# Kernel tuning notes

Hardware: AMD Instinct MI355X
Metric: run time of the kernel (lower is better)

The kernel has to match this reference:

```python
import jax, jax.numpy as jnp
import numpy as np

B, NP, NV, E = 256, 500, 50, 128
FP, FV = 16, 16
DEG_P, DEG_V = 6, 4


def setup_inputs() -> dict:
    key = jax.random.key(0)
    ks = jax.random.split(key, 16)
    rng = np.random.default_rng(0)

    def edges(nb, n, deg):
        per = deg * n
        off = np.repeat(np.arange(nb, dtype=np.int32) * n, per)
        ei = off[None, :] + rng.integers(0, n, size=(2, nb * per)).astype(np.int32)
        return jnp.asarray(ei)

    inp = {
        "p_x": jax.random.normal(ks[0], (B * NP, FP), jnp.float32),
        "v_x": jax.random.normal(ks[1], (B * NV, FV), jnp.float32),
        "p_edge_index": edges(B, NP, DEG_P),
        "v_edge_index": edges(B, NV, DEG_V),
        "p_batch": jnp.asarray(np.repeat(np.arange(B, dtype=np.int32), NP)),
        "v_batch": jnp.asarray(np.repeat(np.arange(B, dtype=np.int32), NV)),
    }

    def lin(k, fi, fo):
        s = 1.0 / np.sqrt(fi)
        kw, kb = jax.random.split(k)
        return (jax.random.uniform(kw, (fi, fo), jnp.float32, -s, s),
                jax.random.uniform(kb, (fo,), jnp.float32, -s, s))

    layers = [("pW0", "pb0", FP, E), ("pW1", "pb1", E, E), ("pW2", "pb2", E, E),
              ("vW0", "vb0", FV, E), ("vW1", "vb1", E, E), ("vW2", "vb2", E, E),
              ("hW1", "hb1", 4 * E, 2 * E), ("hW2", "hb2", 2 * E, E), ("hW3", "hb3", E, 1)]
    for j, (wn, bn, fi, fo) in enumerate(layers):
        W, b = lin(ks[2 + j], fi, fo)
        inp[wn] = W
        inp[bn] = b
    return inp


def _gcn(h, src, dst, dinv, W, b):
    # GCNConv: out[i] = sum_{j->i} dinv[j]*dinv[i] * (h[j] @ W) + dinv[i]^2 * (h[i] @ W) + b
    xw = h @ W
    msg = xw[src] * (dinv[src] * dinv[dst])[:, None]
    agg = jax.ops.segment_sum(msg, dst, num_segments=h.shape[0])
    return agg + xw * (dinv * dinv)[:, None] + b


def _encoder(x, edge_index, batch, W0, b0, W1, b1, W2, b2, nb, npg):
    N = x.shape[0]
    src, dst = edge_index[0], edge_index[1]
    h0 = x @ W0 + b0                                   # node_init_embeddings [N, E]
    ones_e = jnp.ones(src.shape[0], x.dtype)
    deg = 1.0 + jax.ops.segment_sum(ones_e, dst, num_segments=N)  # includes self loop
    dinv = jax.lax.rsqrt(deg)
    h = jax.nn.relu(_gcn(h0, src, dst, dinv, W1, b1))
    h = _gcn(h, src, dst, dinv, W2, b2)                # node_embeddings [N, E]
    counts = jax.ops.segment_sum(jnp.ones(N, x.dtype), batch, num_segments=nb)
    graph = jax.ops.segment_sum(h, batch, num_segments=nb) / counts[:, None]  # [nb, E]
    hd = h.reshape(nb, npg, -1)                        # to_dense_batch (equal-size graphs)
    h0d = h0.reshape(nb, npg, -1)
    gr = jnp.broadcast_to(graph[:, None, :], hd.shape)
    concat = jnp.concatenate([hd, h0d, gr], axis=-1)   # [nb, npg, 3E]
    mask = jnp.ones((nb, npg), bool)
    return graph, concat, mask


def reference(p_x, v_x, p_edge_index, v_edge_index, p_batch, v_batch,
              pW0, pb0, pW1, pb1, pW2, pb2,
              vW0, vb0, vW1, vb1, vW2, vb2,
              hW1, hb1, hW2, hb2, hW3, hb3):
    p_graph, _, _ = _encoder(p_x, p_edge_index, p_batch, pW0, pb0, pW1, pb1, pW2, pb2, B, NP)
    _, v_concat, v_mask = _encoder(v_x, v_edge_index, v_batch, vW0, vb0, vW1, vb1, vW2, vb2, B, NV)
    pg_rep = jnp.broadcast_to(p_graph[:, None, :], (B, NV, p_graph.shape[-1]))
    x = jnp.concatenate([v_concat, pg_rep], axis=-1)   # [B, NV, 4E]
    h = jax.nn.leaky_relu(x @ hW1 + hb1)
    h = jax.nn.leaky_relu(h @ hW2 + hb2)
    logits = (h @ hW3 + hb3)[..., 0]                   # [B, NV]
    return jnp.where(v_mask, logits, jnp.float32(-1e9))
```

## Files before the change

kernel.cpp:

```cpp
#include <hip/hip_runtime.h>
#include <hip/hip_bf16.h>

#define NP_TOT 128000
#define NV_TOT 12800
#define EP_EDGES 768000
#define EV_EDGES 51200
#define NB 256
#define PEPG 3000
#define VEPG 200
#define VCAP 24
#define PITCHV 138

typedef short bf16x8 __attribute__((ext_vector_type(8)));
typedef float f32x4 __attribute__((ext_vector_type(4)));

static __device__ __forceinline__ unsigned short f2bf(float f) {
    unsigned u = __builtin_bit_cast(unsigned, f);
    unsigned r = u + 0x7FFFu + ((u >> 16) & 1u);
    return (unsigned short)(r >> 16);
}
static __device__ __forceinline__ float bf2f(unsigned short h) {
    return __builtin_bit_cast(float, (unsigned)h << 16);
}

static __device__ __forceinline__ void frag_elem(const float* __restrict__ W,
                                                 short* __restrict__ Fh,
                                                 short* __restrict__ Fl,
                                                 int K, int M, int e) {
    if (e >= K * M) return;
    int col = e % M, kk = e / M;
    int ks = kk >> 5, rem = kk & 31, fq = rem >> 3, j = rem & 7;
    float v = W[(size_t)kk * M + col];
    unsigned short h = f2bf(v);
    size_t dst = (((size_t)col * (K >> 5) + ks) * 4 + fq) * 8 + j;
    Fh[dst] = (short)h;
    Fl[dst] = (short)f2bf(v - bf2f(h));
}

__global__ __launch_bounds__(256) void prep_k(
    const float* __restrict__ pW0, const float* __restrict__ pb0,
    const float* __restrict__ pW1,
    float* __restrict__ W01, float* __restrict__ b01,
    const float* __restrict__ vW1, short* __restrict__ W1vh, short* __restrict__ W1vl,
    const float* __restrict__ vW2, short* __restrict__ W2vh, short* __restrict__ W2vl,
    const float* __restrict__ hW1, short* __restrict__ H1h, short* __restrict__ H1l,
    const float* __restrict__ hW2, short* __restrict__ H2h, short* __restrict__ H2l) {
    int bid = blockIdx.x, t = threadIdx.x;
    if (bid == 0) {
        if (t < 128) {
            int col = t;
            float acc[17];
            #pragma unroll
            for (int r = 0; r < 17; r++) acc[r] = 0.f;
            for (int i = 0; i < 128; i++) {
                float w1 = pW1[i * 128 + col];
                #pragma unroll
                for (int r = 0; r < 16; r++) acc[r] += pW0[r * 128 + i] * w1;
                acc[16] += pb0[i] * w1;
            }
            #pragma unroll
            for (int r = 0; r < 16; r++) W01[r * 128 + col] = acc[r];
            b01[col] = acc[16];
        }
    } else if (bid < 65) {
        frag_elem(vW1, W1vh, W1vl, 128, 128, (bid - 1) * 256 + t);
    } else if (bid < 129) {
        frag_elem(vW2, W2vh, W2vl, 128, 128, (bid - 65) * 256 + t);
    } else if (bid < 641) {
        frag_elem(hW1, H1h, H1l, 512, 256, (bid - 129) * 256 + t);
    } else {
        frag_elem(hW2, H2h, H2l, 256, 128, (bid - 641) * 256 + t);
    }
}

__global__ __launch_bounds__(512) void pfused3(const float* __restrict__ x,
                                               const int* __restrict__ ei,
                                               const float* __restrict__ W01,
                                               const float* __restrict__ b01,
                                               const float* __restrict__ b1,
                                               float* __restrict__ p_gz) {
    __shared__ char lds[77824];
    float* sx = (float*)lds;
    unsigned short* sadj = (unsigned short*)(lds + 34816);
    char*  zb    = lds + 59392;
    float* sdinv = (float*)(lds + 69632);
    int*   scnt  = (int*)(lds + 71680);
    float* sbeta = (float*)(lds + 73728);
    float* scsum = (float*)(lds + 75776);

    const int t = threadIdx.x;
    const int b = blockIdx.x;

    scnt[t] = 0; scsum[t] = 0.f;
    const float4* x4 = (const float4*)(x + (size_t)b * 500 * 16);
    for (int i = t; i < 2000; i += 512) {
        float4 v = x4[i];
        int n = i >> 2, q = i & 3;
        float* dst = &sx[n * 17 + q * 4];
        dst[0] = v.x; dst[1] = v.y; dst[2] = v.z; dst[3] = v.w;
    }
    __syncthreads();

    const int* esrc = ei + (size_t)b * PEPG;
    const int* edst = ei + EP_EDGES + (size_t)b * PEPG;
    const int base = b * 500;

    for (int e = t; e < PEPG; e += 512) {
        int s = esrc[e] - base, d = edst[e] - base;
        int slot = atomicAdd(&scnt[d], 1);
        if (slot < VCAP) sadj[d * VCAP + slot] = (unsigned short)s;
    }
    __syncthreads();
    sdinv[t] = rsqrtf(1.0f + (float)scnt[t]);
    __syncthreads();

    for (int e = t; e < PEPG; e += 512)
        atomicAdd(&scsum[esrc[e] - base], sdinv[edst[e] - base]);
    __syncthreads();
    scsum[t] = (t < 500) ? sdinv[t] * (sdinv[t] + scsum[t]) * (1.0f / 500.0f) : 0.f;

    const int lane = t & 63;
    const int wvi = t >> 6;
    const int fr = lane & 15;
    const int fq = lane >> 4;
    const int col = wvi * 16 + fr;
    bf16x8 B1, B2;
    {
        float wt[8];
        #pragma unroll
        for (int j = 0; j < 8; j++)
            wt[j] = W01[(size_t)((fq * 8 + j) & 15) * 128 + col];
        short b1a[8], b2a[8];
        #pragma unroll
        for (int j = 0; j < 8; j++) {
            int kk = fq * 8 + j;
            unsigned short h = f2bf(wt[j]);
            b1a[j] = (short)h;
            b2a[j] = (kk < 16) ? (short)f2bf(wt[j] - bf2f(h)) : (short)0;
        }
        B1 = (bf16x8){b1a[0],b1a[1],b1a[2],b1a[3],b1a[4],b1a[5],b1a[6],b1a[7]};
        B2 = (bf16x8){b2a[0],b2a[1],b2a[2],b2a[3],b2a[4],b2a[5],b2a[6],b2a[7]};
    }
    float b01c = b01[col];
    float b1c = b1[col];
    float pools = 0.f;

    const int cg = t & 7, nb_ = t >> 3, c0 = cg * 2;
    #pragma unroll
    for (int ch = 0; ch < 4; ch++) {
        __syncthreads();
        #pragma unroll
        for (int pass = 0; pass < 2; pass++) {
            int n = ch * 128 + pass * 64 + nb_;
            char* zr = zb + (pass * 64 + nb_) * 80 + cg * 4;
            if (n < 500) {
                float di = sdinv[n];
                int d = scnt[n]; if (d > VCAP) d = VCAP;
                const unsigned short* ap = sadj + n * VCAP;
                float a0 = 0.f, a1 = 0.f, ts = 0.f;
                for (int e = 0; e < d; e++) {
                    int jl = ap[e];
                    float dj = sdinv[jl];
                    a0 += dj * sx[jl * 17 + c0];
                    a1 += dj * sx[jl * 17 + c0 + 1];
                    ts += dj;
                }
                float z0 = di * (di * sx[n * 17 + c0] + a0);
                float z1 = di * (di * sx[n * 17 + c0 + 1] + a1);
                unsigned short h0 = f2bf(z0), h1 = f2bf(z1);
                unsigned short l0 = f2bf(z0 - bf2f(h0)), l1 = f2bf(z1 - bf2f(h1));
                *(unsigned*)(zr)      = (unsigned)h0 | ((unsigned)h1 << 16);
                *(unsigned*)(zr + 32) = (unsigned)l0 | ((unsigned)l1 << 16);
                if (cg == 0) sbeta[n] = di * (di + ts);
            } else {
                *(unsigned*)(zr) = 0u;
                *(unsigned*)(zr + 32) = 0u;
                if (cg == 0) sbeta[n] = 0.f;
            }
        }
        __syncthreads();
        f32x4 acc[8];
        #pragma unroll
        for (int m = 0; m < 8; m++) acc[m] = (f32x4){0.f, 0.f, 0.f, 0.f};
        #pragma unroll
        for (int m = 0; m < 8; m++) {
            int rl = m * 16 + fr;
            bf16x8 a = *(bf16x8*)(zb + rl * 80 + fq * 16);
            acc[m] = __builtin_amdgcn_mfma_f32_16x16x32_bf16(a, B1, acc[m], 0, 0, 0);
            acc[m] = __builtin_amdgcn_mfma_f32_16x16x32_bf16(a, B2, acc[m], 0, 0, 0);
        }
        #pragma unroll
        for (int m = 0; m < 8; m++)
            #pragma unroll
            for (int j = 0; j < 4; j++) {
                int rl = ch * 128 + m * 16 + fq * 4 + j;
                float v = fmaxf(acc[m][j] + sbeta[rl] * b01c + b1c, 0.f);
                pools += scsum[rl] * v;
            }
    }
    pools += __shfl_xor(pools, 16);
    pools += __shfl_xor(pools, 32);
    if (fq == 0) p_gz[(size_t)b * 128 + col] = pools;
}

#define LB 0
#define LC 35328
#define LD 68096
#define LE 100864
#define E_SDINV (LE)
#define E_SCNT  (LE + 256)
#define E_SADJ  (LE + 512)
#define E_SVG   (LE + 5376)
#define E_VGH   (LE + 5888)
#define E_VGL   (LE + 6144)
#define E_PGH   (LE + 6400)
#define E_PGL   (LE + 6656)
#define E_WSUM  (LE + 6912)
__global__ __launch_bounds__(512) void vhead_k(
    const float* __restrict__ v_x,
    const int* __restrict__ v_ei,
    const float* __restrict__ W0, const float* __restrict__ b0,
    const short* __restrict__ W1h, const short* __restrict__ W1l,
    const float* __restrict__ b1,
    const short* __restrict__ W2h, const short* __restrict__ W2l,
    const float* __restrict__ b2,
    const float* __restrict__ p_gz,
    const float* __restrict__ pW2, const float* __restrict__ pb2,
    const short* __restrict__ H1h, const short* __restrict__ H1l,
    const float* __restrict__ hb1,
    const short* __restrict__ H2h, const short* __restrict__ H2l,
    const float* __restrict__ hb2,
    const float* __restrict__ w3, const float* __restrict__ b3,
    float* __restrict__ out) {
    __shared__ char lds[109824];
    const int t = threadIdx.x;
    const int b = blockIdx.x;
    const int lane = t & 63;
    const int wv = t >> 6;
    const int fr = lane & 15;
    const int fq = lane >> 4;
    float* Bf = (float*)(lds + LB);
    float* sdinv = (float*)(lds + E_SDINV);
    int*   scnt  = (int*)(lds + E_SCNT);
    int*   sadj  = (int*)(lds + E_SADJ);

    if (t < 64) scnt[t] = 0;
    *(float4*)(lds + LC + t * 16) = *((const float4*)W0 + t);
    {
        int col = t & 127, q = t >> 7;
        const float* gz = p_gz + (size_t)b * 128;
        float s = 0.f;
        #pragma unroll
        for (int k = 0; k < 32; k++)
            s += gz[q * 32 + k] * pW2[(size_t)(q * 32 + k) * 128 + col];
        ((float*)(lds + E_WSUM))[q * 128 + col] = s;
    }
    __syncthreads();

    if (t < VEPG) {
        int s = v_ei[b * VEPG + t] - b * 50;
        int d = v_ei[EV_EDGES + b * VEPG + t] - b * 50;
        int slot = atomicAdd(&scnt[d], 1);
        if (slot < VCAP) sadj[d * VCAP + slot] = s;
    }
    __syncthreads();

    if (t < 64)
        sdinv[t] = (t < 50) ? rsqrtf(1.0f + (float)scnt[t]) : 0.f;
    if (t < 128) {
        float* part = (float*)(lds + E_WSUM);
        float v = part[t] + part[128 + t] + part[256 + t] + part[384 + t] + pb2[t];
        unsigned short h = f2bf(v);
        ((short*)(lds + E_PGH))[t] = (short)h;
        ((short*)(lds + E_PGL))[t] = (short)f2bf(v - bf2f(h));
    }
    {
        int n = t >> 3, cg = t & 7;
        if (n < 50) {
            const float* sW0 = (const float*)(lds + LC);
            const float4* xr = (const float4*)(v_x + (size_t)(b * 50 + n) * 16);
            float4 x0 = xr[0], x1 = xr[1], x2 = xr[2], x3 = xr[3];
            float xv[16] = {x0.x,x0.y,x0.z,x0.w, x1.x,x1.y,x1.z,x1.w,
                            x2.x,x2.y,x2.z,x2.w, x3.x,x3.y,x3.z,x3.w};
            #pragma unroll
            for (int cc = 0; cc < 16; cc++) {
                int c = cg + cc * 8;
                float a = b0[c];
                #pragma unroll
                for (int k = 0; k < 16; k++) a += xv[k] * sW0[k * 128 + c];
                Bf[n * PITCHV + c] = a;
            }
        }
    }
    __syncthreads();

    {
        #pragma unroll
        for (int g = 0; g < 8; g++) {
            int r = g * 8 + wv;
            float2 v = *(const float2*)&Bf[r * PITCHV + 2 * lane];
            unsigned short h0 = f2bf(v.x), h1 = f2bf(v.y);
            unsigned short l0 = f2bf(v.x - bf2f(h0)), l1 = f2bf(v.y - bf2f(h1));
            int q = (256 + 4 * lane) ^ ((r & 7) << 4);
            *(unsigned*)(lds + LC + r * 512 + q) = (unsigned)h0 | ((unsigned)h1 << 16);
            *(unsigned*)(lds + LD + r * 512 + q) = (unsigned)l0 | ((unsigned)l1 << 16);
        }
        for (int g = 0; g < 7; g++) {
            int n = g * 8 + wv;
            if (n < 50) {
                float di = sdinv[n];
                int d = scnt[n]; if (d > VCAP) d = VCAP;
                const int* ap = sadj + n * VCAP;
                float2 a = *(const float2*)&Bf[n * PITCHV + 2 * lane];
                a.x *= di; a.y *= di;
                for (int e = 0; e < d; e++) {
                    int jl = ap[e];
                    float dj = sdinv[jl];
                    float2 v = *(const float2*)&Bf[jl * PITCHV + 2 * lane];
                    a.x += dj * v.x; a.y += dj * v.y;
                }
                float z0 = di * a.x, z1 = di * a.y;
                unsigned short h0 = f2bf(z0), h1 = f2bf(z1);
                unsigned short l0 = f2bf(z0 - bf2f(h0)), l1 = f2bf(z1 - bf2f(h1));
                int q = (4 * lane) ^ ((n & 7) << 4);
                *(unsigned*)(lds + LC + n * 512 + q) = (unsigned)h0 | ((unsigned)h1 << 16);
                *(unsigned*)(lds + LD + n * 512 + q) = (unsigned)l0 | ((unsigned)l1 << 16);
            }
        }
    }
    __syncthreads();

    {
        const int col = wv * 16 + fr;
        bf16x8 bh[4], bl[4];
        #pragma unroll
        for (int ks = 0; ks < 4; ks++) {
            int base = ((col * 4 + ks) * 4 + fq) * 8;
            bh[ks] = *(const bf16x8*)&W1h[base];
            bl[ks] = *(const bf16x8*)&W1l[base];
        }
        f32x4 acc[4];
        #pragma unroll
        for (int m = 0; m < 4; m++) acc[m] = (f32x4){0.f,0.f,0.f,0.f};
        #pragma unroll
        for (int ks = 0; ks < 4; ks++) {
            int kb = ks * 64 + fq * 16;
            #pragma unroll
            for (int m = 0; m < 4; m++) {
                int r = m * 16 + fr;
                int off = r * 512 + (kb ^ ((r & 7) << 4));
                bf16x8 ah = *(bf16x8*)(lds + LC + off);
                bf16x8 al = *(bf16x8*)(lds + LD + off);
                acc[m] = __builtin_amdgcn_mfma_f32_16x16x32_bf16(ah, bh[ks], acc[m], 0, 0, 0);
                acc[m] = __builtin_amdgcn_mfma_f32_16x16x32_bf16(ah, bl[ks], acc[m], 0, 0, 0);
                acc[m] = __builtin_amdgcn_mfma_f32_16x16x32_bf16(al, bh[ks], acc[m], 0, 0, 0);
            }
        }
        float b1c = b1[col];
        #pragma unroll
        for (int m = 0; m < 4; m++)
            #pragma unroll
            for (int j = 0; j < 4; j++) {
                int row = m * 16 + fq * 4 + j;
                Bf[row * PITCHV + col] = fmaxf(acc[m][j] + b1c, 0.f);
            }
    }
    __syncthreads();

    {
        for (int g = 0; g < 7; g++) {
            int n = g * 8 + wv;
            if (n < 50) {
                float di = sdinv[n];
                int d = scnt[n]; if (d > VCAP) d = VCAP;
                const int* ap = sadj + n * VCAP;
                float2 a = *(const float2*)&Bf[n * PITCHV + 2 * lane];
                a.x *= di; a.y *= di;
                for (int e = 0; e < d; e++) {
                    int jl = ap[e];
                    float dj = sdinv[jl];
                    float2 v = *(const float2*)&Bf[jl * PITCHV + 2 * lane];
                    a.x += dj * v.x; a.y += dj * v.y;
                }
                float z0 = di * a.x, z1 = di * a.y;
                unsigned short h0 = f2bf(z0), h1 = f2bf(z1);
                unsigned short l0 = f2bf(z0 - bf2f(h0)), l1 = f2bf(z1 - bf2f(h1));
                int q = (4 * lane) ^ ((n & 7) << 4);
                *(unsigned*)(lds + LC + n * 512 + q) = (unsigned)h0 | ((unsigned)h1 << 16);
                *(unsigned*)(lds + LD + n * 512 + q) = (unsigned)l0 | ((unsigned)l1 << 16);
            }
        }
    }
    __syncthreads();

    float h2v[4][4];
    {
        const int col = wv * 16 + fr;
        bf16x8 bh[4], bl[4];
        #pragma unroll
        for (int ks = 0; ks < 4; ks++) {
            int base = ((col * 4 + ks) * 4 + fq) * 8;
            bh[ks] = *(const bf16x8*)&W2h[base];
            bl[ks] = *(const bf16x8*)&W2l[base];
        }
        f32x4 acc[4];
        #pragma unroll
        for (int m = 0; m < 4; m++) acc[m] = (f32x4){0.f,0.f,0.f,0.f};
        #pragma unroll
        for (int ks = 0; ks < 4; ks++) {
            int kb = ks * 64 + fq * 16;
            #pragma unroll
            for (int m = 0; m < 4; m++) {
                int r = m * 16 + fr;
                int off = r * 512 + (kb ^ ((r & 7) << 4));
                bf16x8 ah = *(bf16x8*)(lds + LC + off);
                bf16x8 al = *(bf16x8*)(lds + LD + off);
                acc[m] = __builtin_amdgcn_mfma_f32_16x16x32_bf16(ah, bh[ks], acc[m], 0, 0, 0);
                acc[m] = __builtin_amdgcn_mfma_f32_16x16x32_bf16(ah, bl[ks], acc[m], 0, 0, 0);
                acc[m] = __builtin_amdgcn_mfma_f32_16x16x32_bf16(al, bh[ks], acc[m], 0, 0, 0);
            }
        }
        float b2c = b2[col];
        #pragma unroll
        for (int m = 0; m < 4; m++)
            #pragma unroll
            for (int j = 0; j < 4; j++) h2v[m][j] = acc[m][j] + b2c;
    }
    __syncthreads();

    {
        const int col = wv * 16 + fr;
        float s = 0.f;
        #pragma unroll
        for (int m = 0; m < 4; m++)
            #pragma unroll
            for (int j = 0; j < 4; j++) {
                int row = m * 16 + fq * 4 + j;
                float v = h2v[m][j];
                unsigned short h = f2bf(v);
                unsigned short l = f2bf(v - bf2f(h));
                int q = (2 * col) ^ ((row & 7) << 4);
                *(short*)(lds + LC + row * 512 + q) = (short)h;
                *(short*)(lds + LD + row * 512 + q) = (short)l;
                if (row < 50) s += v;
            }
        s += __shfl_xor(s, 16); s += __shfl_xor(s, 32);
        if (fq == 0) ((float*)(lds + E_SVG))[col] = s * (1.0f / 50.0f);
    }
    __syncthreads();

    if (t < 128) {
        float v = ((float*)(lds + E_SVG))[t];
        unsigned short h = f2bf(v);
        ((short*)(lds + E_VGH))[t] = (short)h;
        ((short*)(lds + E_VGL))[t] = (short)f2bf(v - bf2f(h));
    }
    __syncthreads();

    f32x4 accT[4][2];
    #pragma unroll
    for (int m = 0; m < 4; m++)
        #pragma unroll
        for (int nf = 0; nf < 2; nf++) accT[m][nf] = (f32x4){0.f,0.f,0.f,0.f};
    {
        #pragma unroll
        for (int ks = 0; ks < 16; ks++) {
            bf16x8 bh[2], bl[2];
            #pragma unroll
            for (int nf = 0; nf < 2; nf++) {
                int col2 = wv * 32 + nf * 16 + fr;
                int base = ((col2 * 16 + ks) * 4 + fq) * 8;
                bh[nf] = *(const bf16x8*)&H1h[base];
                bl[nf] = *(const bf16x8*)&H1l[base];
            }
            if (ks < 8) {
                int kb = ks * 64 + fq * 16;
                #pragma unroll
                for (int m = 0; m < 4; m++) {
                    int r = m * 16 + fr;
                    int off = r * 512 + (kb ^ ((r & 7) << 4));
                    bf16x8 ah = *(bf16x8*)(lds + LC + off);
                    bf16x8 al = *(bf16x8*)(lds + LD + off);
                    #pragma unroll
                    for (int nf = 0; nf < 2; nf++) {
                        accT[m][nf] = __builtin_amdgcn_mfma_f32_16x16x32_bf16(ah, bh[nf], accT[m][nf], 0, 0, 0);
                        accT[m][nf] = __builtin_amdgcn_mfma_f32_16x16x32_bf16(ah, bl[nf], accT[m][nf], 0, 0, 0);
                        accT[m][nf] = __builtin_amdgcn_mfma_f32_16x16x32_bf16(al, bh[nf], accT[m][nf], 0, 0, 0);
                    }
                }
            } else {
                int boff = (ks < 12) ? (E_VGH + (ks - 8) * 64 + fq * 16)
                                     : (E_PGH + (ks - 12) * 64 + fq * 16);
                int loff = boff + 256;
                bf16x8 ah = *(bf16x8*)(lds + boff);
                bf16x8 al = *(bf16x8*)(lds + loff);
                #pragma unroll
                for (int m = 0; m < 4; m++)
                    #pragma unroll
                    for (int nf = 0; nf < 2; nf++) {
                        accT[m][nf] = __builtin_amdgcn_mfma_f32_16x16x32_bf16(ah, bh[nf], accT[m][nf], 0, 0, 0);
                        accT[m][nf] = __builtin_amdgcn_mfma_f32_16x16x32_bf16(ah, bl[nf], accT[m][nf], 0, 0, 0);
                        accT[m][nf] = __builtin_amdgcn_mfma_f32_16x16x32_bf16(al, bh[nf], accT[m][nf], 0, 0, 0);
                    }
            }
        }
    }
    __syncthreads();
    {
        #pragma unroll
        for (int nf = 0; nf < 2; nf++) {
            int col2 = wv * 32 + nf * 16 + fr;
            float hc = hb1[col2];
            #pragma unroll
            for (int m = 0; m < 4; m++)
                #pragma unroll
                for (int j = 0; j < 4; j++) {
                    int row = m * 16 + fq * 4 + j;
                    float v = accT[m][nf][j] + hc;
                    v = v > 0.f ? v : 0.01f * v;
                    unsigned short h = f2bf(v);
                    unsigned short l = f2bf(v - bf2f(h));
                    int q = (2 * col2) ^ ((row & 7) << 4);
                    *(short*)(lds + LC + row * 512 + q) = (short)h;
                    *(short*)(lds + LD + row * 512 + q) = (short)l;
                }
        }
    }
    __syncthreads();

    {
        const int col3 = wv * 16 + fr;
        f32x4 acc[4];
        #pragma unroll
        for (int m = 0; m < 4; m++) acc[m] = (f32x4){0.f,0.f,0.f,0.f};
        #pragma unroll
        for (int ks = 0; ks < 8; ks++) {
            int base = ((col3 * 8 + ks) * 4 + fq) * 8;
            bf16x8 bh = *(const bf16x8*)&H2h[base];
            bf16x8 bl = *(const bf16x8*)&H2l[base];
            int kb = ks * 64 + fq * 16;
            #pragma unroll
            for (int m = 0; m < 4; m++) {
                int r = m * 16 + fr;
                int off = r * 512 + (kb ^ ((r & 7) << 4));
                bf16x8 ah = *(bf16x8*)(lds + LC + off);
                bf16x8 al = *(bf16x8*)(lds + LD + off);
                acc[m] = __builtin_amdgcn_mfma_f32_16x16x32_bf16(ah, bh, acc[m], 0, 0, 0);
                acc[m] = __builtin_amdgcn_mfma_f32_16x16x32_bf16(ah, bl, acc[m], 0, 0, 0);
                acc[m] = __builtin_amdgcn_mfma_f32_16x16x32_bf16(al, bh, acc[m], 0, 0, 0);
            }
        }
        float hc = hb2[col3], wc = w3[col3];
        float p[4][4];
        #pragma unroll
        for (int m = 0; m < 4; m++)
            #pragma unroll
            for (int j = 0; j < 4; j++) {
                float v = acc[m][j] + hc;
                v = v > 0.f ? v : 0.01f * v;
                p[m][j] = v * wc;
            }
        #pragma unroll
        for (int m = 0; m < 4; m++)
            #pragma unroll
            for (int j = 0; j < 4; j++) {
                p[m][j] += __shfl_xor(p[m][j], 1);
                p[m][j] += __shfl_xor(p[m][j], 2);
                p[m][j] += __shfl_xor(p[m][j], 4);
                p[m][j] += __shfl_xor(p[m][j], 8);
            }
        if (fr == 0) {
            float* wsum = (float*)(lds + E_WSUM);
            #pragma unroll
            for (int m = 0; m < 4; m++)
                #pragma unroll
                for (int j = 0; j < 4; j++)
                    wsum[wv * 64 + m * 16 + fq * 4 + j] = p[m][j];
        }
    }
    __syncthreads();
    if (t < 50) {
        float* wsum = (float*)(lds + E_WSUM);
        float s = 0.f;
        #pragma unroll
        for (int w8 = 0; w8 < 8; w8++) s += wsum[w8 * 64 + t];
        out[b * 50 + t] = s + b3[0];
    }
}

extern "C" void kernel_launch(void* const* d_in, const int* in_sizes, int n_in,
                              void* d_out, int out_size, void* d_ws, size_t ws_size,
                              hipStream_t stream) {
    const float* p_x = (const float*)d_in[0];
    const float* v_x = (const float*)d_in[1];
    const int* p_ei = (const int*)d_in[2];
    const int* v_ei = (const int*)d_in[3];
    const float* pW0 = (const float*)d_in[6];  const float* pb0 = (const float*)d_in[7];
    const float* pW1 = (const float*)d_in[8];  const float* pb1 = (const float*)d_in[9];
    const float* pW2 = (const float*)d_in[10]; const float* pb2 = (const float*)d_in[11];
    const float* vW0 = (const float*)d_in[12]; const float* vb0 = (const float*)d_in[13];
    const float* vW1 = (const float*)d_in[14]; const float* vb1 = (const float*)d_in[15];
    const float* vW2 = (const float*)d_in[16]; const float* vb2 = (const float*)d_in[17];
    const float* hW1 = (const float*)d_in[18]; const float* hb1 = (const float*)d_in[19];
    const float* hW2 = (const float*)d_in[20]; const float* hb2 = (const float*)d_in[21];
    const float* hW3 = (const float*)d_in[22]; const float* hb3 = (const float*)d_in[23];

    char* w = (char*)d_ws;
    size_t off = 0;
    auto alloc = [&](size_t bytes) { char* p = w + off; off += (bytes + 255) & ~size_t(255); return p; };
    float* p_gz = (float*)alloc((size_t)NB * 128 * 4);
    float* W01  = (float*)alloc((size_t)16 * 128 * 4);
    float* b01  = (float*)alloc((size_t)128 * 4);
    short* W1vh = (short*)alloc((size_t)128 * 128 * 2);
    short* W1vl = (short*)alloc((size_t)128 * 128 * 2);
    short* W2vh = (short*)alloc((size_t)128 * 128 * 2);
    short* W2vl = (short*)alloc((size_t)128 * 128 * 2);
    short* H1h  = (short*)alloc((size_t)512 * 256 * 2);
    short* H1l  = (short*)alloc((size_t)512 * 256 * 2);
    short* H2h  = (short*)alloc((size_t)256 * 128 * 2);
    short* H2l  = (short*)alloc((size_t)256 * 128 * 2);

    prep_k<<<769, 256, 0, stream>>>(pW0, pb0, pW1, W01, b01,
                                    vW1, W1vh, W1vl, vW2, W2vh, W2vl,
                                    hW1, H1h, H1l, hW2, H2h, H2l);
    pfused3<<<NB, 512, 0, stream>>>(p_x, p_ei, W01, b01, pb1, p_gz);
    vhead_k<<<NB, 512, 0, stream>>>(v_x, v_ei,
                                    vW0, vb0, W1vh, W1vl, vb1, W2vh, W2vl, vb2,
                                    p_gz, pW2, pb2, H1h, H1l, hb1, H2h, H2l, hb2,
                                    hW3, hb3, (float*)d_out);
}
```

Measured before the change: 83.04 us.

## Double block size to 1024 threads and split MFMA row tiles across wave halves

```diff
diff --git a/kernel.cpp b/kernel.cpp
--- a/kernel.cpp
+++ b/kernel.cpp
@@ -73,13 +73,13 @@
     }
 }
 
-__global__ __launch_bounds__(512) void pfused3(const float* __restrict__ x,
-                                               const int* __restrict__ ei,
-                                               const float* __restrict__ W01,
-                                               const float* __restrict__ b01,
-                                               const float* __restrict__ b1,
-                                               float* __restrict__ p_gz) {
-    __shared__ char lds[77824];
+__global__ __launch_bounds__(1024) void pfused3(const float* __restrict__ x,
+                                                const int* __restrict__ ei,
+                                                const float* __restrict__ W01,
+                                                const float* __restrict__ b01,
+                                                const float* __restrict__ b1,
+                                                float* __restrict__ p_gz) {
+    __shared__ char lds[78848];
     float* sx = (float*)lds;
     unsigned short* sadj = (unsigned short*)(lds + 34816);
     char*  zb    = lds + 59392;
@@ -87,13 +87,14 @@
     int*   scnt  = (int*)(lds + 71680);
     float* sbeta = (float*)(lds + 73728);
     float* scsum = (float*)(lds + 75776);
+    float* pp    = (float*)(lds + 77824);
 
     const int t = threadIdx.x;
     const int b = blockIdx.x;
 
-    scnt[t] = 0; scsum[t] = 0.f;
+    if (t < 512) { scnt[t] = 0; scsum[t] = 0.f; }
     const float4* x4 = (const float4*)(x + (size_t)b * 500 * 16);
-    for (int i = t; i < 2000; i += 512) {
+    for (int i = t; i < 2000; i += 1024) {
         float4 v = x4[i];
         int n = i >> 2, q = i & 3;
         float* dst = &sx[n * 17 + q * 4];
@@ -105,25 +106,27 @@
     const int* edst = ei + EP_EDGES + (size_t)b * PEPG;
     const int base = b * 500;
 
-    for (int e = t; e < PEPG; e += 512) {
+    for (int e = t; e < PEPG; e += 1024) {
         int s = esrc[e] - base, d = edst[e] - base;
         int slot = atomicAdd(&scnt[d], 1);
         if (slot < VCAP) sadj[d * VCAP + slot] = (unsigned short)s;
     }
     __syncthreads();
-    sdinv[t] = rsqrtf(1.0f + (float)scnt[t]);
-    __syncthreads();
-
-    for (int e = t; e < PEPG; e += 512)
+    if (t < 512) sdinv[t] = rsqrtf(1.0f + (float)scnt[t]);
+    __syncthreads();
+
+    for (int e = t; e < PEPG; e += 1024)
         atomicAdd(&scsum[esrc[e] - base], sdinv[edst[e] - base]);
     __syncthreads();
-    scsum[t] = (t < 500) ? sdinv[t] * (sdinv[t] + scsum[t]) * (1.0f / 500.0f) : 0.f;
+    if (t < 512)
+        scsum[t] = (t < 500) ? sdinv[t] * (sdinv[t] + scsum[t]) * (1.0f / 500.0f) : 0.f;
 
     const int lane = t & 63;
     const int wvi = t >> 6;
     const int fr = lane & 15;
     const int fq = lane >> 4;
-    const int col = wvi * 16 + fr;
+    const int col = (wvi & 7) * 16 + fr;
+    const int mh = (wvi >> 3) * 4;
     bf16x8 B1, B2;
     {
         float wt[8];
@@ -149,10 +152,9 @@
     #pragma unroll
     for (int ch = 0; ch < 4; ch++) {
         __syncthreads();
-        #pragma unroll
-        for (int pass = 0; pass < 2; pass++) {
-            int n = ch * 128 + pass * 64 + nb_;
-            char* zr = zb + (pass * 64 + nb_) * 80 + cg * 4;
+        {
+            int n = ch * 128 + nb_;
+            char* zr = zb + nb_ * 80 + cg * 4;
             if (n < 500) {
                 float di = sdinv[n];
                 int d = scnt[n]; if (d > VCAP) d = VCAP;
@@ -179,28 +181,30 @@
             }
         }
         __syncthreads();
-        f32x4 acc[8];
-        #pragma unroll
-        for (int m = 0; m < 8; m++) acc[m] = (f32x4){0.f, 0.f, 0.f, 0.f};
-        #pragma unroll
-        for (int m = 0; m < 8; m++) {
-            int rl = m * 16 + fr;
+        f32x4 acc[4];
+        #pragma unroll
+        for (int m = 0; m < 4; m++) acc[m] = (f32x4){0.f, 0.f, 0.f, 0.f};
+        #pragma unroll
+        for (int m = 0; m < 4; m++) {
+            int rl = (mh + m) * 16 + fr;
             bf16x8 a = *(bf16x8*)(zb + rl * 80 + fq * 16);
             acc[m] = __builtin_amdgcn_mfma_f32_16x16x32_bf16(a, B1, acc[m], 0, 0, 0);
             acc[m] = __builtin_amdgcn_mfma_f32_16x16x32_bf16(a, B2, acc[m], 0, 0, 0);
         }
         #pragma unroll
-        for (int m = 0; m < 8; m++)
+        for (int m = 0; m < 4; m++)
             #pragma unroll
             for (int j = 0; j < 4; j++) {
-                int rl = ch * 128 + m * 16 + fq * 4 + j;
+                int rl = ch * 128 + (mh + m) * 16 + fq * 4 + j;
                 float v = fmaxf(acc[m][j] + sbeta[rl] * b01c + b1c, 0.f);
                 pools += scsum[rl] * v;
             }
     }
     pools += __shfl_xor(pools, 16);
     pools += __shfl_xor(pools, 32);
-    if (fq == 0) p_gz[(size_t)b * 128 + col] = pools;
+    if (fq == 0) pp[(wvi >> 3) * 128 + col] = pools;
+    __syncthreads();
+    if (t < 128) p_gz[(size_t)b * 128 + t] = pp[t] + pp[128 + t];
 }
 
 #define LB 0
@@ -211,12 +215,12 @@
 #define E_SCNT  (LE + 256)
 #define E_SADJ  (LE + 512)
 #define E_SVG   (LE + 5376)
-#define E_VGH   (LE + 5888)
-#define E_VGL   (LE + 6144)
-#define E_PGH   (LE + 6400)
-#define E_PGL   (LE + 6656)
-#define E_WSUM  (LE + 6912)
-__global__ __launch_bounds__(512) void vhead_k(
+#define E_VGH   (LE + 6400)
+#define E_VGL   (LE + 6656)
+#define E_PGH   (LE + 6912)
+#define E_PGL   (LE + 7168)
+#define E_WSUM  (LE + 7424)
+__global__ __launch_bounds__(1024) void vhead_k(
     const float* __restrict__ v_x,
     const int* __restrict__ v_ei,
     const float* __restrict__ W0, const float* __restrict__ b0,
@@ -232,7 +236,7 @@
     const float* __restrict__ hb2,
     const float* __restrict__ w3, const float* __restrict__ b3,
     float* __restrict__ out) {
-    __shared__ char lds[109824];
+    __shared__ char lds[112384];
     const int t = threadIdx.x;
     const int b = blockIdx.x;
     const int lane = t & 63;
@@ -245,8 +249,8 @@
     int*   sadj  = (int*)(lds + E_SADJ);
 
     if (t < 64) scnt[t] = 0;
-    *(float4*)(lds + LC + t * 16) = *((const float4*)W0 + t);
-    {
+    if (t < 512) *(float4*)(lds + LC + t * 16) = *((const float4*)W0 + t);
+    if (t < 512) {
         int col = t & 127, q = t >> 7;
         const float* gz = p_gz + (size_t)b * 128;
         float s = 0.f;
@@ -296,8 +300,8 @@
 
     {
         #pragma unroll
-        for (int g = 0; g < 8; g++) {
-            int r = g * 8 + wv;
+        for (int g = 0; g < 4; g++) {
+            int r = g * 16 + wv;
             float2 v = *(const float2*)&Bf[r * PITCHV + 2 * lane];
             unsigned short h0 = f2bf(v.x), h1 = f2bf(v.y);
             unsigned short l0 = f2bf(v.x - bf2f(h0)), l1 = f2bf(v.y - bf2f(h1));
@@ -305,8 +309,8 @@
             *(unsigned*)(lds + LC + r * 512 + q) = (unsigned)h0 | ((unsigned)h1 << 16);
             *(unsigned*)(lds + LD + r * 512 + q) = (unsigned)l0 | ((unsigned)l1 << 16);
         }
-        for (int g = 0; g < 7; g++) {
-            int n = g * 8 + wv;
+        for (int g = 0; g < 4; g++) {
+            int n = g * 16 + wv;
             if (n < 50) {
                 float di = sdinv[n];
                 int d = scnt[n]; if (d > VCAP) d = VCAP;
@@ -331,7 +335,8 @@
     __syncthreads();
 
     {
-        const int col = wv * 16 + fr;
+        const int col = (wv & 7) * 16 + fr;
+        const int mh = (wv >> 3) * 2;
         bf16x8 bh[4], bl[4];
         #pragma unroll
         for (int ks = 0; ks < 4; ks++) {
@@ -339,37 +344,37 @@
             bh[ks] = *(const bf16x8*)&W1h[base];
             bl[ks] = *(const bf16x8*)&W1l[base];
         }
-        f32x4 acc[4];
-        #pragma unroll
-        for (int m = 0; m < 4; m++) acc[m] = (f32x4){0.f,0.f,0.f,0.f};
+        f32x4 acc[2];
+        acc[0] = (f32x4){0.f,0.f,0.f,0.f};
+        acc[1] = (f32x4){0.f,0.f,0.f,0.f};
         #pragma unroll
         for (int ks = 0; ks < 4; ks++) {
             int kb = ks * 64 + fq * 16;
             #pragma unroll
-            for (int m = 0; m < 4; m++) {
-                int r = m * 16 + fr;
+            for (int m2 = 0; m2 < 2; m2++) {
+                int r = (mh + m2) * 16 + fr;
                 int off = r * 512 + (kb ^ ((r & 7) << 4));
                 bf16x8 ah = *(bf16x8*)(lds + LC + off);
                 bf16x8 al = *(bf16x8*)(lds + LD + off);
-                acc[m] = __builtin_amdgcn_mfma_f32_16x16x32_bf16(ah, bh[ks], acc[m], 0, 0, 0);
-                acc[m] = __builtin_amdgcn_mfma_f32_16x16x32_bf16(ah, bl[ks], acc[m], 0, 0, 0);
-                acc[m] = __builtin_amdgcn_mfma_f32_16x16x32_bf16(al, bh[ks], acc[m], 0, 0, 0);
+                acc[m2] = __builtin_amdgcn_mfma_f32_16x16x32_bf16(ah, bh[ks], acc[m2], 0, 0, 0);
+                acc[m2] = __builtin_amdgcn_mfma_f32_16x16x32_bf16(ah, bl[ks], acc[m2], 0, 0, 0);
+                acc[m2] = __builtin_amdgcn_mfma_f32_16x16x32_bf16(al, bh[ks], acc[m2], 0, 0, 0);
             }
         }
         float b1c = b1[col];
         #pragma unroll
-        for (int m = 0; m < 4; m++)
+        for (int m2 = 0; m2 < 2; m2++)
             #pragma unroll
             for (int j = 0; j < 4; j++) {
-                int row = m * 16 + fq * 4 + j;
-                Bf[row * PITCHV + col] = fmaxf(acc[m][j] + b1c, 0.f);
-            }
-    }
-    __syncthreads();
-
-    {
-        for (int g = 0; g < 7; g++) {
-            int n = g * 8 + wv;
+                int row = (mh + m2) * 16 + fq * 4 + j;
+                Bf[row * PITCHV + col] = fmaxf(acc[m2][j] + b1c, 0.f);
+            }
+    }
+    __syncthreads();
+
+    {
+        for (int g = 0; g < 4; g++) {
+            int n = g * 16 + wv;
             if (n < 50) {
                 float di = sdinv[n];
                 int d = scnt[n]; if (d > VCAP) d = VCAP;
@@ -393,9 +398,10 @@
     }
     __syncthreads();
 
-    float h2v[4][4];
-    {
-        const int col = wv * 16 + fr;
+    float h2v[2][4];
+    {
+        const int col = (wv & 7) * 16 + fr;
+        const int mh = (wv >> 3) * 2;
         bf16x8 bh[4], bl[4];
         #pragma unroll
         for (int ks = 0; ks < 4; ks++) {
@@ -403,40 +409,41 @@
             bh[ks] = *(const bf16x8*)&W2h[base];
             bl[ks] = *(const bf16x8*)&W2l[base];
         }
-        f32x4 acc[4];
-        #pragma unroll
-        for (int m = 0; m < 4; m++) acc[m] = (f32x4){0.f,0.f,0.f,0.f};
+        f32x4 acc[2];
+        acc[0] = (f32x4){0.f,0.f,0.f,0.f};
+        acc[1] = (f32x4){0.f,0.f,0.f,0.f};
         #pragma unroll
         for (int ks = 0; ks < 4; ks++) {
             int kb = ks * 64 + fq * 16;
             #pragma unroll
-            for (int m = 0; m < 4; m++) {
-                int r = m * 16 + fr;
+            for (int m2 = 0; m2 < 2; m2++) {
+                int r = (mh + m2) * 16 + fr;
                 int off = r * 512 + (kb ^ ((r & 7) << 4));
                 bf16x8 ah = *(bf16x8*)(lds + LC + off);
                 bf16x8 al = *(bf16x8*)(lds + LD + off);
-                acc[m] = __builtin_amdgcn_mfma_f32_16x16x32_bf16(ah, bh[ks], acc[m], 0, 0, 0);
-                acc[m] = __builtin_amdgcn_mfma_f32_16x16x32_bf16(ah, bl[ks], acc[m], 0, 0, 0);
-                acc[m] = __builtin_amdgcn_mfma_f32_16x16x32_bf16(al, bh[ks], acc[m], 0, 0, 0);
+                acc[m2] = __builtin_amdgcn_mfma_f32_16x16x32_bf16(ah, bh[ks], acc[m2], 0, 0, 0);
+                acc[m2] = __builtin_amdgcn_mfma_f32_16x16x32_bf16(ah, bl[ks], acc[m2], 0, 0, 0);
+                acc[m2] = __builtin_amdgcn_mfma_f32_16x16x32_bf16(al, bh[ks], acc[m2], 0, 0, 0);
             }
         }
         float b2c = b2[col];
         #pragma unroll
-        for (int m = 0; m < 4; m++)
-            #pragma unroll
-            for (int j = 0; j < 4; j++) h2v[m][j] = acc[m][j] + b2c;
-    }
-    __syncthreads();
-
-    {
-        const int col = wv * 16 + fr;
+        for (int m2 = 0; m2 < 2; m2++)
+            #pragma unroll
+            for (int j = 0; j < 4; j++) h2v[m2][j] = acc[m2][j] + b2c;
+    }
+    __syncthreads();
+
+    {
+        const int col = (wv & 7) * 16 + fr;
+        const int mh = (wv >> 3) * 2;
         float s = 0.f;
         #pragma unroll
-        for (int m = 0; m < 4; m++)
+        for (int m2 = 0; m2 < 2; m2++)
             #pragma unroll
             for (int j = 0; j < 4; j++) {
-                int row = m * 16 + fq * 4 + j;
-                float v = h2v[m][j];
+                int row = (mh + m2) * 16 + fq * 4 + j;
+                float v = h2v[m2][j];
                 unsigned short h = f2bf(v);
                 unsigned short l = f2bf(v - bf2f(h));
                 int q = (2 * col) ^ ((row & 7) << 4);
@@ -445,30 +452,32 @@
                 if (row < 50) s += v;
             }
         s += __shfl_xor(s, 16); s += __shfl_xor(s, 32);
-        if (fq == 0) ((float*)(lds + E_SVG))[col] = s * (1.0f / 50.0f);
+        if (fq == 0) ((float*)(lds + E_SVG))[(wv >> 3) * 128 + col] = s;
     }
     __syncthreads();
 
     if (t < 128) {
-        float v = ((float*)(lds + E_SVG))[t];
+        float* svg = (float*)(lds + E_SVG);
+        float v = (svg[t] + svg[128 + t]) * (1.0f / 50.0f);
         unsigned short h = f2bf(v);
         ((short*)(lds + E_VGH))[t] = (short)h;
         ((short*)(lds + E_VGL))[t] = (short)f2bf(v - bf2f(h));
     }
     __syncthreads();
 
-    f32x4 accT[4][2];
+    f32x4 accT[2][2];
     #pragma unroll
-    for (int m = 0; m < 4; m++)
-        #pragma unroll
-        for (int nf = 0; nf < 2; nf++) accT[m][nf] = (f32x4){0.f,0.f,0.f,0.f};
-    {
+    for (int m2 = 0; m2 < 2; m2++)
+        #pragma unroll
+        for (int nf = 0; nf < 2; nf++) accT[m2][nf] = (f32x4){0.f,0.f,0.f,0.f};
+    {
+        const int mh = (wv >> 3) * 2;
         #pragma unroll
         for (int ks = 0; ks < 16; ks++) {
             bf16x8 bh[2], bl[2];
             #pragma unroll
             for (int nf = 0; nf < 2; nf++) {
-                int col2 = wv * 32 + nf * 16 + fr;
+                int col2 = (wv & 7) * 32 + nf * 16 + fr;
                 int base = ((col2 * 16 + ks) * 4 + fq) * 8;
                 bh[nf] = *(const bf16x8*)&H1h[base];
                 bl[nf] = *(const bf16x8*)&H1l[base];
@@ -476,16 +485,16 @@
             if (ks < 8) {
                 int kb = ks * 64 + fq * 16;
                 #pragma unroll
-                for (int m = 0; m < 4; m++) {
-                    int r = m * 16 + fr;
+                for (int m2 = 0; m2 < 2; m2++) {
+                    int r = (mh + m2) * 16 + fr;
                     int off = r * 512 + (kb ^ ((r & 7) << 4));
                     bf16x8 ah = *(bf16x8*)(lds + LC + off);
                     bf16x8 al = *(bf16x8*)(lds + LD + off);
                     #pragma unroll
                     for (int nf = 0; nf < 2; nf++) {
-                        accT[m][nf] = __builtin_amdgcn_mfma_f32_16x16x32_bf16(ah, bh[nf], accT[m][nf], 0, 0, 0);
-                        accT[m][nf] = __builtin_amdgcn_mfma_f32_16x16x32_bf16(ah, bl[nf], accT[m][nf], 0, 0, 0);
-                        accT[m][nf] = __builtin_amdgcn_mfma_f32_16x16x32_bf16(al, bh[nf], accT[m][nf], 0, 0, 0);
+                        accT[m2][nf] = __builtin_amdgcn_mfma_f32_16x16x32_bf16(ah, bh[nf], accT[m2][nf], 0, 0, 0);
+                        accT[m2][nf] = __builtin_amdgcn_mfma_f32_16x16x32_bf16(ah, bl[nf], accT[m2][nf], 0, 0, 0);
+                        accT[m2][nf] = __builtin_amdgcn_mfma_f32_16x16x32_bf16(al, bh[nf], accT[m2][nf], 0, 0, 0);
                     }
                 }
             } else {
@@ -495,28 +504,29 @@
                 bf16x8 ah = *(bf16x8*)(lds + boff);
                 bf16x8 al = *(bf16x8*)(lds + loff);
                 #pragma unroll
-                for (int m = 0; m < 4; m++)
+                for (int m2 = 0; m2 < 2; m2++)
                     #pragma unroll
                     for (int nf = 0; nf < 2; nf++) {
-                        accT[m][nf] = __builtin_amdgcn_mfma_f32_16x16x32_bf16(ah, bh[nf], accT[m][nf], 0, 0, 0);
-                        accT[m][nf] = __builtin_amdgcn_mfma_f32_16x16x32_bf16(ah, bl[nf], accT[m][nf], 0, 0, 0);
-                        accT[m][nf] = __builtin_amdgcn_mfma_f32_16x16x32_bf16(al, bh[nf], accT[m][nf], 0, 0, 0);
+                        accT[m2][nf] = __builtin_amdgcn_mfma_f32_16x16x32_bf16(ah, bh[nf], accT[m2][nf], 0, 0, 0);
+                        accT[m2][nf] = __builtin_amdgcn_mfma_f32_16x16x32_bf16(ah, bl[nf], accT[m2][nf], 0, 0, 0);
+                        accT[m2][nf] = __builtin_amdgcn_mfma_f32_16x16x32_bf16(al, bh[nf], accT[m2][nf], 0, 0, 0);
                     }
             }
         }
     }
     __syncthreads();
     {
+        const int mh = (wv >> 3) * 2;
         #pragma unroll
         for (int nf = 0; nf < 2; nf++) {
-            int col2 = wv * 32 + nf * 16 + fr;
+            int col2 = (wv & 7) * 32 + nf * 16 + fr;
             float hc = hb1[col2];
             #pragma unroll
-            for (int m = 0; m < 4; m++)
+            for (int m2 = 0; m2 < 2; m2++)
                 #pragma unroll
                 for (int j = 0; j < 4; j++) {
-                    int row = m * 16 + fq * 4 + j;
-                    float v = accT[m][nf][j] + hc;
+                    int row = (mh + m2) * 16 + fq * 4 + j;
+                    float v = accT[m2][nf][j] + hc;
                     v = v > 0.f ? v : 0.01f * v;
                     unsigned short h = f2bf(v);
                     unsigned short l = f2bf(v - bf2f(h));
@@ -529,10 +539,11 @@
     __syncthreads();
 
     {
-        const int col3 = wv * 16 + fr;
-        f32x4 acc[4];
-        #pragma unroll
-        for (int m = 0; m < 4; m++) acc[m] = (f32x4){0.f,0.f,0.f,0.f};
+        const int col3 = (wv & 7) * 16 + fr;
+        const int mh = (wv >> 3) * 2;
+        f32x4 acc[2];
+        acc[0] = (f32x4){0.f,0.f,0.f,0.f};
+        acc[1] = (f32x4){0.f,0.f,0.f,0.f};
         #pragma unroll
         for (int ks = 0; ks < 8; ks++) {
             int base = ((col3 * 8 + ks) * 4 + fq) * 8;
@@ -540,50 +551,51 @@
             bf16x8 bl = *(const bf16x8*)&H2l[base];
             int kb = ks * 64 + fq * 16;
             #pragma unroll
-            for (int m = 0; m < 4; m++) {
-                int r = m * 16 + fr;
+            for (int m2 = 0; m2 < 2; m2++) {
+                int r = (mh + m2) * 16 + fr;
                 int off = r * 512 + (kb ^ ((r & 7) << 4));
                 bf16x8 ah = *(bf16x8*)(lds + LC + off);
                 bf16x8 al = *(bf16x8*)(lds + LD + off);
-                acc[m] = __builtin_amdgcn_mfma_f32_16x16x32_bf16(ah, bh, acc[m], 0, 0, 0);
-                acc[m] = __builtin_amdgcn_mfma_f32_16x16x32_bf16(ah, bl, acc[m], 0, 0, 0);
-                acc[m] = __builtin_amdgcn_mfma_f32_16x16x32_bf16(al, bh, acc[m], 0, 0, 0);
+                acc[m2] = __builtin_amdgcn_mfma_f32_16x16x32_bf16(ah, bh, acc[m2], 0, 0, 0);
+                acc[m2] = __builtin_amdgcn_mfma_f32_16x16x32_bf16(ah, bl, acc[m2], 0, 0, 0);
+                acc[m2] = __builtin_amdgcn_mfma_f32_16x16x32_bf16(al, bh, acc[m2], 0, 0, 0);
             }
         }
         float hc = hb2[col3], wc = w3[col3];
-        float p[4][4];
-        #pragma unroll
-        for (int m = 0; m < 4; m++)
+        float p[2][4];
+        #pragma unroll
+        for (int m2 = 0; m2 < 2; m2++)
             #pragma unroll
             for (int j = 0; j < 4; j++) {
-                float v = acc[m][j] + hc;
+                float v = acc[m2][j] + hc;
                 v = v > 0.f ? v : 0.01f * v;
-                p[m][j] = v * wc;
-            }
-        #pragma unroll
-        for (int m = 0; m < 4; m++)
+                p[m2][j] = v * wc;
+            }
+        #pragma unroll
+        for (int m2 = 0; m2 < 2; m2++)
             #pragma unroll
             for (int j = 0; j < 4; j++) {
-                p[m][j] += __shfl_xor(p[m][j], 1);
-                p[m][j] += __shfl_xor(p[m][j], 2);
-                p[m][j] += __shfl_xor(p[m][j], 4);
-                p[m][j] += __shfl_xor(p[m][j], 8);
+                p[m2][j] += __shfl_xor(p[m2][j], 1);
+                p[m2][j] += __shfl_xor(p[m2][j], 2);
+                p[m2][j] += __shfl_xor(p[m2][j], 4);
+                p[m2][j] += __shfl_xor(p[m2][j], 8);
             }
         if (fr == 0) {
             float* wsum = (float*)(lds + E_WSUM);
             #pragma unroll
-            for (int m = 0; m < 4; m++)
+            for (int m2 = 0; m2 < 2; m2++)
                 #pragma unroll
                 for (int j = 0; j < 4; j++)
-                    wsum[wv * 64 + m * 16 + fq * 4 + j] = p[m][j];
+                    wsum[wv * 64 + (mh + m2) * 16 + fq * 4 + j] = p[m2][j];
         }
     }
     __syncthreads();
     if (t < 50) {
         float* wsum = (float*)(lds + E_WSUM);
+        int g0 = (t >= 32) ? 8 : 0;
         float s = 0.f;
         #pragma unroll
-        for (int w8 = 0; w8 < 8; w8++) s += wsum[w8 * 64 + t];
+        for (int k = 0; k < 8; k++) s += wsum[(g0 + k) * 64 + t];
         out[b * 50 + t] = s + b3[0];
     }
 }
@@ -623,9 +635,9 @@
     prep_k<<<769, 256, 0, stream>>>(pW0, pb0, pW1, W01, b01,
                                     vW1, W1vh, W1vl, vW2, W2vh, W2vl,
                                     hW1, H1h, H1l, hW2, H2h, H2l);
-    pfused3<<<NB, 512, 0, stream>>>(p_x, p_ei, W01, b01, pb1, p_gz);
-    vhead_k<<<NB, 512, 0, stream>>>(v_x, v_ei,
-                                    vW0, vb0, W1vh, W1vl, vb1, W2vh, W2vl, vb2,
-                                    p_gz, pW2, pb2, H1h, H1l, hb1, H2h, H2l, hb2,
-                                    hW3, hb3, (float*)d_out);
+    pfused3<<<NB, 1024, 0, stream>>>(p_x, p_ei, W01, b01, pb1, p_gz);
+    vhead_k<<<NB, 1024, 0, stream>>>(v_x, v_ei,
+                                     vW0, vb0, W1vh, W1vl, vb1, W2vh, W2vl, vb2,
+                                     p_gz, pW2, pb2, H1h, H1l, hb1, H2h, H2l, hb2,
+                                     hW3, hb3, (float*)d_out);
 }
```

Measured after the change: 105.3 us. +26.9%, slower.
